# Performance work log

Hardware: AMD Instinct MI355X
Metric: run time of the kernel (lower is better)

## Reference

```python
import jax, jax.numpy as jnp
import numpy as np

OUTPUT_DIM = 64
HIDDEN = 1024
STYLE = 128
SKILL = 128
SEQ_LEN = 256
N_LAYERS = 2
BATCH = 512


def setup_inputs() -> dict:
    key = jax.random.key(0)
    ks = jax.random.split(key, 16)
    s = 0.02
    inp = {
        "z_style": jax.random.normal(ks[0], (BATCH, STYLE), jnp.float32),
        "z_skill": jax.random.normal(ks[1], (BATCH, SKILL), jnp.float32),
        "fc_init_w": jax.random.normal(ks[2], (HIDDEN * N_LAYERS, STYLE + SKILL), jnp.float32) * s,
        "fc_init_b": jnp.zeros((HIDDEN * N_LAYERS,), jnp.float32),
        "W_ih0": jax.random.normal(ks[3], (4 * HIDDEN, OUTPUT_DIM), jnp.float32) * s,
        "W_hh0": jax.random.normal(ks[4], (4 * HIDDEN, HIDDEN), jnp.float32) * s,
        "b_ih0": jnp.zeros((4 * HIDDEN,), jnp.float32),
        "b_hh0": jnp.zeros((4 * HIDDEN,), jnp.float32),
        "W_ih1": jax.random.normal(ks[5], (4 * HIDDEN, HIDDEN), jnp.float32) * s,
        "W_hh1": jax.random.normal(ks[6], (4 * HIDDEN, HIDDEN), jnp.float32) * s,
        "b_ih1": jnp.zeros((4 * HIDDEN,), jnp.float32),
        "b_hh1": jnp.zeros((4 * HIDDEN,), jnp.float32),
        "fc_out_w": jax.random.normal(ks[7], (OUTPUT_DIM, HIDDEN), jnp.float32) * s,
        "fc_out_b": jnp.zeros((OUTPUT_DIM,), jnp.float32),
    }
    return inp


def _lstm_cell(x, h, c, W_ih, W_hh, b_ih, b_hh):
    # PyTorch gate order: i, f, g, o
    gates = x @ W_ih.T + b_ih + h @ W_hh.T + b_hh  # [B, 4H]
    i, f, g, o = jnp.split(gates, 4, axis=-1)
    i = jax.nn.sigmoid(i)
    f = jax.nn.sigmoid(f)
    g = jnp.tanh(g)
    o = jax.nn.sigmoid(o)
    c_new = f * c + i * g
    h_new = o * jnp.tanh(c_new)
    return h_new, c_new


def reference(z_style, z_skill, fc_init_w, fc_init_b, W_ih0, W_hh0, b_ih0, b_hh0,
              W_ih1, W_hh1, b_ih1, b_hh1, fc_out_w, fc_out_b):
    z = jnp.concatenate([z_style, z_skill], axis=1)                # [B, STYLE+SKILL]
    init_flat = z @ fc_init_w.T + fc_init_b                        # [B, n_layers*H]
    # Faithful to torch .view: raw row-major reshape to [n_layers, B, H]
    h0_all = init_flat.reshape(N_LAYERS, -1, HIDDEN)
    c0_all = jnp.zeros_like(h0_all)
    x0 = jnp.zeros((z.shape[0], OUTPUT_DIM), z.dtype)

    def step(carry, _):
        h0, c0, h1, c1, x = carry
        h0, c0 = _lstm_cell(x, h0, c0, W_ih0, W_hh0, b_ih0, b_hh0)
        h1, c1 = _lstm_cell(h0, h1, c1, W_ih1, W_hh1, b_ih1, b_hh1)
        out = h1 @ fc_out_w.T + fc_out_b                           # [B, OUTPUT_DIM]
        return (h0, c0, h1, c1, out), out

    carry0 = (h0_all[0], c0_all[0], h0_all[1], c0_all[1], x0)
    _, outs = jax.lax.scan(step, carry0, None, length=SEQ_LEN)     # [T, B, OUT]
    return jnp.transpose(outs, (1, 0, 2))                          # [B, T, OUT]
```

## Files before the change

### kernel.cpp

```cpp
#include <hip/hip_runtime.h>
#include <hip/hip_bf16.h>
#include <hip/hip_cooperative_groups.h>

#define HID   1024
#define BATCH 512
#define SEQ   256
#define OUTD  64
#define NGATE 4096
#define NBLK  256
#define NTHR  512
#define NPH   512
#define HSZ   (512 * 1024)

typedef __attribute__((ext_vector_type(8))) short bf16x8;
typedef __attribute__((ext_vector_type(4))) float f32x4;
typedef __attribute__((ext_vector_type(16))) float f32x16;
typedef unsigned short u16;
typedef unsigned long long u64;

#define WIN_BYTES 32768
#define LDS_BYTES (2 * WIN_BYTES + 65536)

#define AQ __ATOMIC_RELAXED, __HIP_MEMORY_SCOPE_AGENT

__device__ __forceinline__ u16 f2bf(float v) {
  union { float f; unsigned u; } u; u.f = v;
  unsigned r = u.u + 0x7fffu + ((u.u >> 16) & 1u);
  return (u16)(r >> 16);
}
__device__ __forceinline__ float bf2f(u16 b) {
  union { unsigned u; float f; } u; u.u = ((unsigned)b) << 16;
  return u.f;
}
__device__ __forceinline__ float sigf(float x) { return 1.0f / (1.0f + __expf(-x)); }
__device__ __forceinline__ float tanh_fast(float x) {
  float ax = fabsf(x);
  float e = __expf(-2.0f * ax);
  return copysignf((1.0f - e) / (1.0f + e), x);
}

__device__ __forceinline__ void st_dev32(u16* p, unsigned v) {
  __hip_atomic_store((unsigned*)p, v, AQ);
}
__device__ __forceinline__ u64 ld_dev64(const u16* p) {
  return __hip_atomic_load((const u64*)p, AQ);
}

__device__ __forceinline__ size_t fidx(int np, int k) {
  int s = np >> 5, nl = np & 31;
  int c = k >> 8;
  int kq = (k >> 5) & 7;
  int kfs = (k >> 4) & 1;
  int h = (k >> 3) & 1;
  int e = k & 7;
  int f = c * 2 + kfs;
  return ((size_t)(s * 8 + kq) * 16 + f) * 512 + (h * 32 + nl) * 8 + e;
}


__global__ void k_build_w0f(const float* __restrict__ Whh0, const float* __restrict__ Wih0,
                            const float* __restrict__ fcw, u16* __restrict__ w0f) {
  int np = blockIdx.x;
  int j = np >> 2, gg = np & 3;
  int orig = gg * 1024 + j;
  int tid = threadIdx.x;
  __shared__ float wrow[64];
  if (tid < 64) wrow[tid] = Wih0[orig * 64 + tid];
  __syncthreads();
  for (int k = tid; k < 1024; k += 256) {
    w0f[fidx(np, k)] = f2bf(Whh0[(size_t)orig * 1024 + k]);
    float acc = 0.f;
#pragma unroll
    for (int o = 0; o < 64; ++o) acc += wrow[o] * fcw[o * 1024 + k];
    w0f[fidx(np, 1024 + k)] = f2bf(acc);
  }
}

__global__ void k_build_w1f(const float* __restrict__ Wih1, const float* __restrict__ Whh1,
                            u16* __restrict__ w1f) {
  int np = blockIdx.x;
  int j = np >> 2, gg = np & 3;
  int orig = gg * 1024 + j;
  int tid = threadIdx.x;
  for (int k = tid; k < 1024; k += 256) {
    w1f[fidx(np, k)]        = f2bf(Wih1[(size_t)orig * 1024 + k]);
    w1f[fidx(np, 1024 + k)] = f2bf(Whh1[(size_t)orig * 1024 + k]);
  }
}

__global__ void k_build_bias(const float* bih0, const float* bhh0,
                             const float* bih1, const float* bhh1,
                             const float* Wih0, const float* fcb,
                             float* bias0b, float* bias0x, float* bias1) {
  int np = blockIdx.x * 256 + threadIdx.x;
  if (np >= NGATE) return;
  int j = np >> 2, gg = np & 3;
  int orig = gg * 1024 + j;
  bias0b[np] = bih0[orig] + bhh0[orig];
  bias1[np]  = bih1[orig] + bhh1[orig];
  float acc = 0.f;
#pragma unroll
  for (int o = 0; o < 64; ++o) acc += Wih0[orig * 64 + o] * fcb[o];
  bias0x[np] = acc;
}

__global__ void k_fcwb(const float* __restrict__ fcw, u16* __restrict__ fcwb) {
  int idx = blockIdx.x * 256 + threadIdx.x;
  fcwb[idx] = f2bf(fcw[idx]);
}

__global__ void k_init(const float* __restrict__ zs, const float* __restrict__ zk,
                       const float* __restrict__ fiw, const float* __restrict__ fib,
                       u16* __restrict__ xg0i, u16* __restrict__ xg1i) {
  int r = blockIdx.x;
  int tid = threadIdx.x;
  __shared__ float z[256];
  if (tid < 128) z[tid] = zs[r * 128 + tid];
  else           z[tid] = zk[r * 128 + (tid - 128)];
  __syncthreads();
  for (int c = tid; c < 2048; c += 256) {
    float acc = fib[c];
    const float* w = fiw + (size_t)c * 256;
#pragma unroll 8
    for (int k = 0; k < 256; ++k) acc += z[k] * w[k];
    int l = (r >= 256) ? 1 : 0;
    int b = 2 * (r - l * 256) + (c >> 10);
    int h = c & 1023;
    u16 v = f2bf(acc);
    if (l == 0) xg0i[(size_t)b * 1024 + h] = v;
    else        xg1i[(size_t)b * 1024 + h] = v;
  }
}


struct Params {
  const u16* w0f;
  const u16* w1f;
  const float* bias0b;
  const float* bias0x;
  const float* bias1;
  u16* xg0;
  u16* xg1;
  u16* scr;
  const u16* fcwb;
  const float* fcb;
  float* out;
  unsigned* igctr;
  unsigned* rkg;
  unsigned* gcnt;
  unsigned* sctr;
  unsigned* axg;
  unsigned* rls;
  unsigned* gctr;
};

__global__ __launch_bounds__(NTHR, 2)
void k_lstm(Params p) {
  extern __shared__ char smem[];
  u16* win0 = (u16*)smem;
  u16* win1 = (u16*)(smem + WIN_BYTES);
  float* pld = (float*)(smem + 2 * WIN_BYTES);
  volatile unsigned* bc = (volatile unsigned*)pld;

  const int blk = blockIdx.x, tid = threadIdx.x;
  const int lane = tid & 63, wave = tid >> 6;
  const int x8 = blk & 7;
  const int g = x8 >> 2;
  const int s = (blk >> 3) * 4 + (x8 & 3);
  const int nl = lane & 31, hh = lane >> 5;

  unsigned xcd;
  asm("s_getreg_b32 %0, hwreg(HW_REG_XCC_ID, 0, 32)" : "=s"(xcd));
  xcd &= 7;

  if (tid == 0) {
    unsigned rg = __hip_atomic_fetch_add(&p.rkg[xcd * 2 + g], 1u, AQ);
    __hip_atomic_fetch_add(&p.gcnt[g], 1u, AQ);
    __hip_atomic_fetch_add(p.igctr, 1u, AQ);
    while (__hip_atomic_load(p.igctr, AQ) < (unsigned)NBLK)
      __builtin_amdgcn_s_sleep(2);
    bc[0] = rg;
    bc[1] = __hip_atomic_load(&p.rkg[xcd * 2 + g], AQ);
    bc[2] = __hip_atomic_load(&p.gcnt[g], AQ);
  }
  __syncthreads();
  const unsigned rg_   = bc[0];
  const unsigned ng_   = bc[1];
  const unsigned ngrp_ = bc[2];
  const bool lead = (rg_ == 0);
  __syncthreads();

  bf16x8 w0r[16], w1r[16];
  {
    const u16* W0p = p.w0f + (size_t)(s * 8 + wave) * 8192 + (hh * 32 + nl) * 8;
    const u16* W1p = p.w1f + (size_t)(s * 8 + wave) * 8192 + (hh * 32 + nl) * 8;
#pragma unroll
    for (int f = 0; f < 16; ++f) {
      w0r[f] = *(const bf16x8*)(W0p + f * 512);
      w1r[f] = *(const bf16x8*)(W1p + f * 512);
    }
  }

  const int cr_ = tid >> 3, cj = tid & 7;
  const int npb = s * 32 + 4 * cj;
  const f32x4 b0 = *(const f32x4*)&p.bias0b[npb];
  const f32x4 bx = *(const f32x4*)&p.bias0x[npb];
  const f32x4 b1 = *(const f32x4*)&p.bias1[npb];
  const int jcol = s * 8 + cj;

  float c0s[4] = {0, 0, 0, 0}, c1s[4] = {0, 0, 0, 0};

  u16* scrg = p.scr + (size_t)(xcd * 2 + g) * 256 * 2048;

  auto gbar = [&](int ph) {
    __syncthreads();
    if (tid == 0) {
      unsigned* ax = &p.axg[(xcd * 2 + g) * NPH + ph];
      __hip_atomic_fetch_add(ax, 1u, AQ);
      if (lead) {
        while (__hip_atomic_load(ax, AQ) < ng_) __builtin_amdgcn_s_sleep(1);
        unsigned* gc = &p.gctr[g * NPH + ph];
        __hip_atomic_fetch_add(gc, ng_, AQ);
        while (__hip_atomic_load(gc, AQ) < ngrp_) __builtin_amdgcn_s_sleep(1);
        __hip_atomic_store(&p.rls[(xcd * 2 + g) * NPH + ph], 1u, AQ);
      } else {
        while (!__hip_atomic_load(&p.rls[(xcd * 2 + g) * NPH + ph], AQ))
          __builtin_amdgcn_s_sleep(1);
      }
    }
    __syncthreads();
  };

  auto lbar = [&](int ph) {
    __syncthreads();
    if (tid == 0) {
      unsigned* c = &p.sctr[(xcd * 2 + g) * NPH + ph];
      __hip_atomic_fetch_add(c, 1u, AQ);
      while (__hip_atomic_load(c, AQ) < ng_) __builtin_amdgcn_s_sleep(1);
    }
    __syncthreads();
    asm volatile("buffer_inv sc0\n\ts_waitcnt vmcnt(0)" ::: "memory");
  };

  auto fill = [&](const u16* lo, const u16* hi, bool zhi, bool dohi) {
    const int c = tid;
    for (int r = (int)rg_; r < 256; r += (int)ng_) {
      u16* drow = scrg + (size_t)r * 2048;
      const size_t grow = (size_t)(g * 256 + r) * 1024;
      if (c < 256) {
        *(u64*)(drow + c * 4) = ld_dev64(lo + grow + c * 4);
      } else if (dohi) {
        *(u64*)(drow + 1024 + (c - 256) * 4) =
            zhi ? 0ull : ld_dev64(hi + grow + (c - 256) * 4);
      }
    }
  };

  auto out_proj_s = [&](int tq) {
    const int o = tid >> 3, ks = tid & 7;
#pragma unroll
    for (int rr = 0; rr < 2; ++rr) {
      const int rl = 2 * s + rr;
      const u16* hp = scrg + (size_t)rl * 2048 + 1024 + ks * 128;
      const u16* wp = p.fcwb + (size_t)o * 1024 + ks * 128;
      float a = 0.f;
#pragma unroll
      for (int kk = 0; kk < 128; kk += 8) {
        bf16x8 hv = *(const bf16x8*)(hp + kk);
        bf16x8 wv = *(const bf16x8*)(wp + kk);
#pragma unroll
        for (int jj = 0; jj < 8; ++jj)
          a += bf2f(((u16*)&hv)[jj]) * bf2f(((u16*)&wv)[jj]);
      }
      a += __shfl_xor(a, 1);
      a += __shfl_xor(a, 2);
      a += __shfl_xor(a, 4);
      if (ks == 0)
        p.out[((size_t)(g * 256 + rl) * SEQ + tq) * OUTD + o] = a + p.fcb[o];
    }
  };

  auto phase = [&](bf16x8 (&wr)[16], u16* dst,
                   const f32x4& bb, const f32x4& bxx, bool ubx, float (&cs)[4]) {
#pragma unroll
    for (int pass = 0; pass < 4; ++pass) {
      const u16* Xb = scrg + (size_t)(pass * 64) * 2048;
      f32x16 acc0, acc1;
#pragma unroll
      for (int z = 0; z < 16; ++z) { acc0[z] = 0.f; acc1[z] = 0.f; }

      {
        const int row = tid >> 3, seg = tid & 7, sw = (row & 7) << 4;
        const u16* src = Xb + (size_t)row * 2048 + seg * 8;
#pragma unroll
        for (int i = 0; i < 4; ++i)
          *(bf16x8*)(win0 + row * 256 + (((seg * 16 + i * 128) ^ sw) >> 1)) =
              *(const bf16x8*)(src + i * 64);
      }
      __syncthreads();
#pragma unroll
      for (int c = 0; c < 8; ++c) {
        u16* cur = (c & 1) ? win1 : win0;
        u16* nxt = (c & 1) ? win0 : win1;
        if (c < 7) {
          const int row = tid >> 3, seg = tid & 7, sw = (row & 7) << 4;
          const u16* src = Xb + (size_t)row * 2048 + (c + 1) * 256 + seg * 8;
#pragma unroll
          for (int i = 0; i < 4; ++i)
            *(bf16x8*)(nxt + row * 256 + (((seg * 16 + i * 128) ^ sw) >> 1)) =
                *(const bf16x8*)(src + i * 64);
        }
#pragma unroll
        for (int kfs = 0; kfs < 2; ++kfs) {
          const bf16x8 wf = wr[c * 2 + kfs];
          const int bo = wave * 64 + kfs * 32 + hh * 16;
          {
            const int row = nl;
            const bf16x8 a =
                *(const bf16x8*)(cur + row * 256 + ((bo ^ ((row & 7) << 4)) >> 1));
            acc0 = __builtin_amdgcn_mfma_f32_32x32x16_bf16(a, wf, acc0, 0, 0, 0);
          }
          {
            const int row = 32 + nl;
            const bf16x8 a =
                *(const bf16x8*)(cur + row * 256 + ((bo ^ ((row & 7) << 4)) >> 1));
            acc1 = __builtin_amdgcn_mfma_f32_32x32x16_bf16(a, wf, acc1, 0, 0, 0);
          }
        }
        __syncthreads();
      }
#pragma unroll
      for (int r16 = 0; r16 < 16; ++r16) {
        const int row0 = (r16 & 3) + 8 * (r16 >> 2) + 4 * hh;
        pld[(wave * 64 + row0) * 32 + nl] = acc0[r16];
        pld[(wave * 64 + 32 + row0) * 32 + nl] = acc1[r16];
      }
      __syncthreads();
      f32x4 gs = {0.f, 0.f, 0.f, 0.f};
#pragma unroll
      for (int q = 0; q < 8; ++q) {
        const f32x4 v = *(const f32x4*)&pld[(q * 64 + cr_) * 32 + 4 * cj];
        gs[0] += v[0]; gs[1] += v[1]; gs[2] += v[2]; gs[3] += v[3];
      }
      const float gi = gs[0] + bb[0] + (ubx ? bxx[0] : 0.f);
      const float gf = gs[1] + bb[1] + (ubx ? bxx[1] : 0.f);
      const float gg = gs[2] + bb[2] + (ubx ? bxx[2] : 0.f);
      const float go = gs[3] + bb[3] + (ubx ? bxx[3] : 0.f);
      const float iv = sigf(gi), fv = sigf(gf), gv = tanh_fast(gg), ov = sigf(go);
      const float cnew = fv * cs[pass] + iv * gv;
      cs[pass] = cnew;
      const float hnew = ov * tanh_fast(cnew);
      const u16 hv = f2bf(hnew);
      const unsigned other = __shfl_xor((unsigned)hv, 1);
      if (!(tid & 1)) {
        const unsigned pairv = (unsigned)hv | (other << 16);
        st_dev32(dst + (size_t)(g * 256 + pass * 64 + cr_) * 1024 + jcol, pairv);
      }
      __syncthreads();
    }
  };

  for (int t = 0; t < SEQ; ++t) {
    const int pp = t & 1, pq = pp ^ 1;
    const int ph = 2 * t;
    fill(p.xg0 + (size_t)pq * HSZ, p.xg1 + (size_t)pq * HSZ, t == 0, true);
    lbar(ph);
    if (t > 0) out_proj_s(t - 1);
    phase(w0r, p.xg0 + (size_t)pp * HSZ, b0, bx, t > 0, c0s);
    gbar(ph);
    fill(p.xg0 + (size_t)pp * HSZ, p.xg1 + (size_t)pq * HSZ, false, t == 0);
    lbar(ph + 1);
    phase(w1r, p.xg1 + (size_t)pp * HSZ, b1, b1, false, c1s);
    gbar(ph + 1);
  }
  {
    const u16* h1b = p.xg1 + (size_t)((SEQ - 1) & 1) * HSZ;
    const int o = tid >> 3, ks = tid & 7;
#pragma unroll
    for (int rr = 0; rr < 2; ++rr) {
      const int r = g * 256 + 2 * s + rr;
      const u16* hp = h1b + (size_t)r * 1024 + ks * 128;
      const u16* wp = p.fcwb + (size_t)o * 1024 + ks * 128;
      float a = 0.f;
      for (int kk = 0; kk < 128; kk += 4) {
        u64 hv = ld_dev64(hp + kk);
        a += bf2f((u16)hv)         * bf2f(wp[kk]);
        a += bf2f((u16)(hv >> 16)) * bf2f(wp[kk + 1]);
        a += bf2f((u16)(hv >> 32)) * bf2f(wp[kk + 2]);
        a += bf2f((u16)(hv >> 48)) * bf2f(wp[kk + 3]);
      }
      a += __shfl_xor(a, 1);
      a += __shfl_xor(a, 2);
      a += __shfl_xor(a, 4);
      if (ks == 0)
        p.out[((size_t)r * SEQ + (SEQ - 1)) * OUTD + o] = a + p.fcb[o];
    }
  }
}


extern "C" void kernel_launch(void* const* d_in, const int* in_sizes, int n_in,
                              void* d_out, int out_size, void* d_ws, size_t ws_size,
                              hipStream_t stream) {
  const float* zs   = (const float*)d_in[0];
  const float* zk   = (const float*)d_in[1];
  const float* fiw  = (const float*)d_in[2];
  const float* fib  = (const float*)d_in[3];
  const float* Wih0 = (const float*)d_in[4];
  const float* Whh0 = (const float*)d_in[5];
  const float* bih0 = (const float*)d_in[6];
  const float* bhh0 = (const float*)d_in[7];
  const float* Wih1 = (const float*)d_in[8];
  const float* Whh1 = (const float*)d_in[9];
  const float* bih1 = (const float*)d_in[10];
  const float* bhh1 = (const float*)d_in[11];
  const float* fcw  = (const float*)d_in[12];
  const float* fcb  = (const float*)d_in[13];
  float* out = (float*)d_out;

  char* ws = (char*)d_ws;
  size_t off = 0;
  auto alloc = [&](size_t bytes) -> char* {
    char* pp = ws + off;
    off += (bytes + 255) & ~(size_t)255;
    return pp;
  };
  u16* w0f  = (u16*)alloc((size_t)NGATE * 2048 * 2);
  u16* w1f  = (u16*)alloc((size_t)NGATE * 2048 * 2);
  u16* xg0  = (u16*)alloc((size_t)2 * HSZ * 2);
  u16* xg1  = (u16*)alloc((size_t)2 * HSZ * 2);
  u16* scr  = (u16*)alloc((size_t)8 * 2 * 256 * 2048 * 2);
  u16* fcwb = (u16*)alloc((size_t)OUTD * HID * 2);
  float* bias0b = (float*)alloc(NGATE * 4);
  float* bias0x = (float*)alloc(NGATE * 4);
  float* bias1  = (float*)alloc(NGATE * 4);
  unsigned* igctr = (unsigned*)alloc(256);
  unsigned* rkg   = (unsigned*)alloc(16 * 4);
  unsigned* gcnt  = (unsigned*)alloc(2 * 4);
  unsigned* sctr  = (unsigned*)alloc((size_t)16 * NPH * 4);
  unsigned* axg   = (unsigned*)alloc((size_t)16 * NPH * 4);
  unsigned* rls   = (unsigned*)alloc((size_t)16 * NPH * 4);
  unsigned* gctr  = (unsigned*)alloc((size_t)2 * NPH * 4);

  hipMemsetAsync(igctr, 0, 256, stream);
  hipMemsetAsync(rkg, 0, 16 * 4, stream);
  hipMemsetAsync(gcnt, 0, 2 * 4, stream);
  hipMemsetAsync(sctr, 0, (size_t)16 * NPH * 4, stream);
  hipMemsetAsync(axg, 0, (size_t)16 * NPH * 4, stream);
  hipMemsetAsync(rls, 0, (size_t)16 * NPH * 4, stream);
  hipMemsetAsync(gctr, 0, (size_t)2 * NPH * 4, stream);

  hipLaunchKernelGGL(k_build_w0f, dim3(NGATE), dim3(256), 0, stream, Whh0, Wih0, fcw, w0f);
  hipLaunchKernelGGL(k_build_w1f, dim3(NGATE), dim3(256), 0, stream, Wih1, Whh1, w1f);
  hipLaunchKernelGGL(k_build_bias, dim3(16), dim3(256), 0, stream,
                     bih0, bhh0, bih1, bhh1, Wih0, fcb, bias0b, bias0x, bias1);
  hipLaunchKernelGGL(k_fcwb, dim3(256), dim3(256), 0, stream, fcw, fcwb);
  hipLaunchKernelGGL(k_init, dim3(BATCH), dim3(256), 0, stream, zs, zk, fiw, fib,
                     xg0 + (size_t)1 * HSZ, xg1 + (size_t)1 * HSZ);

  Params prm;
  prm.w0f = w0f; prm.w1f = w1f;
  prm.bias0b = bias0b; prm.bias0x = bias0x; prm.bias1 = bias1;
  prm.xg0 = xg0; prm.xg1 = xg1; prm.scr = scr;
  prm.fcwb = fcwb; prm.fcb = fcb; prm.out = out;
  prm.igctr = igctr; prm.rkg = rkg; prm.gcnt = gcnt;
  prm.sctr = sctr; prm.axg = axg; prm.rls = rls; prm.gctr = gctr;

  hipFuncSetAttribute((const void*)k_lstm, hipFuncAttributeMaxDynamicSharedMemorySize, LDS_BYTES);
  void* args[] = { &prm };
  hipLaunchCooperativeKernel((void*)k_lstm, dim3(NBLK), dim3(NTHR), args, LDS_BYTES, stream);
}
```

Measured before the change: 22.23 ms.

## Drop LDS staging windows, read MFMA operands from scratch directly, single-buffer hidden state

Removes the double-buffered LDS window staging in the gate GEMM, so MFMA A-operands are loaded straight from the per-XCD scratch buffer and the per-chunk __syncthreads go away. The hidden-state buffers become single instead of ping-pong, and the fill step is split into per-layer halves using 16-byte loads marked sc0 sc1 with batched waits. The barrier schedule is reordered so each layer refreshes only the half it needs. The risks are higher global/L2 latency on MFMA operand fetches and write-after-read hazards on the now single-buffered state.

```diff
diff --git a/kernel.cpp b/kernel.cpp
--- a/kernel.cpp
+++ b/kernel.cpp
@@ -10,16 +10,17 @@
 #define NBLK  256
 #define NTHR  512
 #define NPH   512
+#define NLB   520
 #define HSZ   (512 * 1024)
 
 typedef __attribute__((ext_vector_type(8))) short bf16x8;
 typedef __attribute__((ext_vector_type(4))) float f32x4;
 typedef __attribute__((ext_vector_type(16))) float f32x16;
+typedef __attribute__((ext_vector_type(4))) unsigned u32x4;
 typedef unsigned short u16;
 typedef unsigned long long u64;
 
-#define WIN_BYTES 32768
-#define LDS_BYTES (2 * WIN_BYTES + 65536)
+#define LDS_BYTES (65536 + 256)
 
 #define AQ __ATOMIC_RELAXED, __HIP_MEMORY_SCOPE_AGENT
 
@@ -45,6 +46,10 @@
 __device__ __forceinline__ u64 ld_dev64(const u16* p) {
   return __hip_atomic_load((const u64*)p, AQ);
 }
+
+#define LD_BYP16(dst, addr) \
+  asm volatile("global_load_dwordx4 %0, %1, off sc0 sc1" \
+               : "=v"(dst) : "v"(addr) : "memory")
 
 __device__ __forceinline__ size_t fidx(int np, int k) {
   int s = np >> 5, nl = np & 31;
@@ -111,7 +116,7 @@
 
 __global__ void k_init(const float* __restrict__ zs, const float* __restrict__ zk,
                        const float* __restrict__ fiw, const float* __restrict__ fib,
-                       u16* __restrict__ xg0i, u16* __restrict__ xg1i) {
+                       u16* __restrict__ xg0, u16* __restrict__ xg1) {
   int r = blockIdx.x;
   int tid = threadIdx.x;
   __shared__ float z[256];
@@ -127,8 +132,8 @@
     int b = 2 * (r - l * 256) + (c >> 10);
     int h = c & 1023;
     u16 v = f2bf(acc);
-    if (l == 0) xg0i[(size_t)b * 1024 + h] = v;
-    else        xg1i[(size_t)b * 1024 + h] = v;
+    if (l == 0) xg0[(size_t)b * 1024 + h] = v;
+    else        xg1[(size_t)b * 1024 + h] = v;
   }
 }
 
@@ -157,10 +162,8 @@
 __global__ __launch_bounds__(NTHR, 2)
 void k_lstm(Params p) {
   extern __shared__ char smem[];
-  u16* win0 = (u16*)smem;
-  u16* win1 = (u16*)(smem + WIN_BYTES);
-  float* pld = (float*)(smem + 2 * WIN_BYTES);
-  volatile unsigned* bc = (volatile unsigned*)pld;
+  float* pld = (float*)smem;
+  volatile unsigned* bc = (volatile unsigned*)(smem + 65536);
 
   const int blk = blockIdx.x, tid = threadIdx.x;
   const int lane = tid & 63, wave = tid >> 6;
@@ -231,10 +234,10 @@
     __syncthreads();
   };
 
-  auto lbar = [&](int ph) {
+  auto lbar = [&](int slot) {
     __syncthreads();
     if (tid == 0) {
-      unsigned* c = &p.sctr[(xcd * 2 + g) * NPH + ph];
+      unsigned* c = &p.sctr[(xcd * 2 + g) * NLB + slot];
       __hip_atomic_fetch_add(c, 1u, AQ);
       while (__hip_atomic_load(c, AQ) < ng_) __builtin_amdgcn_s_sleep(1);
     }
@@ -242,17 +245,25 @@
     asm volatile("buffer_inv sc0\n\ts_waitcnt vmcnt(0)" ::: "memory");
   };
 
-  auto fill = [&](const u16* lo, const u16* hi, bool zhi, bool dohi) {
-    const int c = tid;
-    for (int r = (int)rg_; r < 256; r += (int)ng_) {
-      u16* drow = scrg + (size_t)r * 2048;
-      const size_t grow = (size_t)(g * 256 + r) * 1024;
-      if (c < 256) {
-        *(u64*)(drow + c * 4) = ld_dev64(lo + grow + c * 4);
-      } else if (dohi) {
-        *(u64*)(drow + 1024 + (c - 256) * 4) =
-            zhi ? 0ull : ld_dev64(hi + grow + (c - 256) * 4);
-      }
+  auto fill_half = [&](const u16* src, int off, bool zero) {
+    const int rsub = tid >> 7;
+    const int csub = (tid & 127) * 8;
+    for (int c0 = (int)rg_; c0 < 64; c0 += 4 * (int)ng_) {
+      const int c1 = c0 + (int)ng_, c2 = c0 + 2 * (int)ng_, c3 = c0 + 3 * (int)ng_;
+      u32x4 v0 = {0,0,0,0}, v1 = {0,0,0,0}, v2 = {0,0,0,0}, v3 = {0,0,0,0};
+      if (!zero) {
+        LD_BYP16(v0, src + (size_t)(g * 256 + c0 * 4 + rsub) * 1024 + csub);
+        if (c1 < 64) LD_BYP16(v1, src + (size_t)(g * 256 + c1 * 4 + rsub) * 1024 + csub);
+        if (c2 < 64) LD_BYP16(v2, src + (size_t)(g * 256 + c2 * 4 + rsub) * 1024 + csub);
+        if (c3 < 64) LD_BYP16(v3, src + (size_t)(g * 256 + c3 * 4 + rsub) * 1024 + csub);
+        asm volatile("s_waitcnt vmcnt(0)"
+                     : "+v"(v0), "+v"(v1), "+v"(v2), "+v"(v3) :: "memory");
+        __builtin_amdgcn_sched_barrier(0);
+      }
+      *(u32x4*)(scrg + (size_t)(c0 * 4 + rsub) * 2048 + off + csub) = v0;
+      if (c1 < 64) *(u32x4*)(scrg + (size_t)(c1 * 4 + rsub) * 2048 + off + csub) = v1;
+      if (c2 < 64) *(u32x4*)(scrg + (size_t)(c2 * 4 + rsub) * 2048 + off + csub) = v2;
+      if (c3 < 64) *(u32x4*)(scrg + (size_t)(c3 * 4 + rsub) * 2048 + off + csub) = v3;
     }
   };
 
@@ -284,50 +295,21 @@
                    const f32x4& bb, const f32x4& bxx, bool ubx, float (&cs)[4]) {
 #pragma unroll
     for (int pass = 0; pass < 4; ++pass) {
-      const u16* Xb = scrg + (size_t)(pass * 64) * 2048;
+      const u16* b0p = scrg + (size_t)(pass * 64 + nl) * 2048 + wave * 32 + hh * 8;
+      const u16* b1p = b0p + (size_t)32 * 2048;
       f32x16 acc0, acc1;
 #pragma unroll
       for (int z = 0; z < 16; ++z) { acc0[z] = 0.f; acc1[z] = 0.f; }
-
-      {
-        const int row = tid >> 3, seg = tid & 7, sw = (row & 7) << 4;
-        const u16* src = Xb + (size_t)row * 2048 + seg * 8;
-#pragma unroll
-        for (int i = 0; i < 4; ++i)
-          *(bf16x8*)(win0 + row * 256 + (((seg * 16 + i * 128) ^ sw) >> 1)) =
-              *(const bf16x8*)(src + i * 64);
-      }
-      __syncthreads();
 #pragma unroll
       for (int c = 0; c < 8; ++c) {
-        u16* cur = (c & 1) ? win1 : win0;
-        u16* nxt = (c & 1) ? win0 : win1;
-        if (c < 7) {
-          const int row = tid >> 3, seg = tid & 7, sw = (row & 7) << 4;
-          const u16* src = Xb + (size_t)row * 2048 + (c + 1) * 256 + seg * 8;
-#pragma unroll
-          for (int i = 0; i < 4; ++i)
-            *(bf16x8*)(nxt + row * 256 + (((seg * 16 + i * 128) ^ sw) >> 1)) =
-                *(const bf16x8*)(src + i * 64);
-        }
-#pragma unroll
-        for (int kfs = 0; kfs < 2; ++kfs) {
-          const bf16x8 wf = wr[c * 2 + kfs];
-          const int bo = wave * 64 + kfs * 32 + hh * 16;
-          {
-            const int row = nl;
-            const bf16x8 a =
-                *(const bf16x8*)(cur + row * 256 + ((bo ^ ((row & 7) << 4)) >> 1));
-            acc0 = __builtin_amdgcn_mfma_f32_32x32x16_bf16(a, wf, acc0, 0, 0, 0);
-          }
-          {
-            const int row = 32 + nl;
-            const bf16x8 a =
-                *(const bf16x8*)(cur + row * 256 + ((bo ^ ((row & 7) << 4)) >> 1));
-            acc1 = __builtin_amdgcn_mfma_f32_32x32x16_bf16(a, wf, acc1, 0, 0, 0);
-          }
-        }
-        __syncthreads();
+        const bf16x8 f0 = *(const bf16x8*)(b0p + c * 256);
+        const bf16x8 f1 = *(const bf16x8*)(b0p + c * 256 + 16);
+        const bf16x8 f2 = *(const bf16x8*)(b1p + c * 256);
+        const bf16x8 f3 = *(const bf16x8*)(b1p + c * 256 + 16);
+        acc0 = __builtin_amdgcn_mfma_f32_32x32x16_bf16(f0, wr[2 * c],     acc0, 0, 0, 0);
+        acc0 = __builtin_amdgcn_mfma_f32_32x32x16_bf16(f1, wr[2 * c + 1], acc0, 0, 0, 0);
+        acc1 = __builtin_amdgcn_mfma_f32_32x32x16_bf16(f2, wr[2 * c],     acc1, 0, 0, 0);
+        acc1 = __builtin_amdgcn_mfma_f32_32x32x16_bf16(f3, wr[2 * c + 1], acc1, 0, 0, 0);
       }
 #pragma unroll
       for (int r16 = 0; r16 < 16; ++r16) {
@@ -360,26 +342,30 @@
     }
   };
 
+  fill_half(p.xg0, 0, false);
+  fill_half(nullptr, 1024, true);
+  lbar(0);
+
   for (int t = 0; t < SEQ; ++t) {
-    const int pp = t & 1, pq = pp ^ 1;
-    const int ph = 2 * t;
-    fill(p.xg0 + (size_t)pq * HSZ, p.xg1 + (size_t)pq * HSZ, t == 0, true);
-    lbar(ph);
     if (t > 0) out_proj_s(t - 1);
-    phase(w0r, p.xg0 + (size_t)pp * HSZ, b0, bx, t > 0, c0s);
-    gbar(ph);
-    fill(p.xg0 + (size_t)pp * HSZ, p.xg1 + (size_t)pq * HSZ, false, t == 0);
-    lbar(ph + 1);
-    phase(w1r, p.xg1 + (size_t)pp * HSZ, b1, b1, false, c1s);
-    gbar(ph + 1);
+    phase(w0r, p.xg0, b0, bx, t > 0, c0s);
+    gbar(2 * t);
+    fill_half(p.xg0, 0, false);
+    if (t == 0) fill_half(p.xg1, 1024, false);
+    lbar(2 * t + 1);
+    phase(w1r, p.xg1, b1, b1, false, c1s);
+    gbar(2 * t + 1);
+    if (t + 1 < SEQ) {
+      fill_half(p.xg1, 1024, false);
+      lbar(2 * t + 2);
+    }
   }
   {
-    const u16* h1b = p.xg1 + (size_t)((SEQ - 1) & 1) * HSZ;
     const int o = tid >> 3, ks = tid & 7;
 #pragma unroll
     for (int rr = 0; rr < 2; ++rr) {
       const int r = g * 256 + 2 * s + rr;
-      const u16* hp = h1b + (size_t)r * 1024 + ks * 128;
+      const u16* hp = p.xg1 + (size_t)r * 1024 + ks * 128;
       const u16* wp = p.fcwb + (size_t)o * 1024 + ks * 128;
       float a = 0.f;
       for (int kk = 0; kk < 128; kk += 4) {
@@ -427,8 +413,8 @@
   };
   u16* w0f  = (u16*)alloc((size_t)NGATE * 2048 * 2);
   u16* w1f  = (u16*)alloc((size_t)NGATE * 2048 * 2);
-  u16* xg0  = (u16*)alloc((size_t)2 * HSZ * 2);
-  u16* xg1  = (u16*)alloc((size_t)2 * HSZ * 2);
+  u16* xg0  = (u16*)alloc((size_t)HSZ * 2);
+  u16* xg1  = (u16*)alloc((size_t)HSZ * 2);
   u16* scr  = (u16*)alloc((size_t)8 * 2 * 256 * 2048 * 2);
   u16* fcwb = (u16*)alloc((size_t)OUTD * HID * 2);
   float* bias0b = (float*)alloc(NGATE * 4);
@@ -437,7 +423,7 @@
   unsigned* igctr = (unsigned*)alloc(256);
   unsigned* rkg   = (unsigned*)alloc(16 * 4);
   unsigned* gcnt  = (unsigned*)alloc(2 * 4);
-  unsigned* sctr  = (unsigned*)alloc((size_t)16 * NPH * 4);
+  unsigned* sctr  = (unsigned*)alloc((size_t)16 * NLB * 4);
   unsigned* axg   = (unsigned*)alloc((size_t)16 * NPH * 4);
   unsigned* rls   = (unsigned*)alloc((size_t)16 * NPH * 4);
   unsigned* gctr  = (unsigned*)alloc((size_t)2 * NPH * 4);
@@ -445,7 +431,7 @@
   hipMemsetAsync(igctr, 0, 256, stream);
   hipMemsetAsync(rkg, 0, 16 * 4, stream);
   hipMemsetAsync(gcnt, 0, 2 * 4, stream);
-  hipMemsetAsync(sctr, 0, (size_t)16 * NPH * 4, stream);
+  hipMemsetAsync(sctr, 0, (size_t)16 * NLB * 4, stream);
   hipMemsetAsync(axg, 0, (size_t)16 * NPH * 4, stream);
   hipMemsetAsync(rls, 0, (size_t)16 * NPH * 4, stream);
   hipMemsetAsync(gctr, 0, (size_t)2 * NPH * 4, stream);
@@ -455,8 +441,7 @@
   hipLaunchKernelGGL(k_build_bias, dim3(16), dim3(256), 0, stream,
                      bih0, bhh0, bih1, bhh1, Wih0, fcb, bias0b, bias0x, bias1);
   hipLaunchKernelGGL(k_fcwb, dim3(256), dim3(256), 0, stream, fcw, fcwb);
-  hipLaunchKernelGGL(k_init, dim3(BATCH), dim3(256), 0, stream, zs, zk, fiw, fib,
-                     xg0 + (size_t)1 * HSZ, xg1 + (size_t)1 * HSZ);
+  hipLaunchKernelGGL(k_init, dim3(BATCH), dim3(256), 0, stream, zs, zk, fiw, fib, xg0, xg1);
 
   Params prm;
   prm.w0f = w0f; prm.w1f = w1f;
```

After: 35.65 ms. 1.6x slower.

## Single-buffer hidden states and move layer-1 fill after phase barrier

Applied to the files above, without the earlier changes.

Drops the double-buffered xg0/xg1 hidden-state arrays in favour of single buffers. The per-block scratch fill is restructured so each half is copied right after the phase that produced it, and the fill loop is batched with eight independent loads in flight per thread. This reorders the per-step schedule, so the first fill and local barrier move out of the loop. It also resizes the local-barrier counter array and moves the broadcast LDS slot so it no longer aliases pld. The aim is fewer redundant copies and more memory-level parallelism in the fill, at the risk of read-after-write hazards on the now-shared single buffers.

```diff
diff --git a/kernel.cpp b/kernel.cpp
--- a/kernel.cpp
+++ b/kernel.cpp
@@ -10,6 +10,7 @@
 #define NBLK  256
 #define NTHR  512
 #define NPH   512
+#define NLB   520
 #define HSZ   (512 * 1024)
 
 typedef __attribute__((ext_vector_type(8))) short bf16x8;
@@ -19,7 +20,7 @@
 typedef unsigned long long u64;
 
 #define WIN_BYTES 32768
-#define LDS_BYTES (2 * WIN_BYTES + 65536)
+#define LDS_BYTES (2 * WIN_BYTES + 65536 + 256)
 
 #define AQ __ATOMIC_RELAXED, __HIP_MEMORY_SCOPE_AGENT
 
@@ -111,7 +112,7 @@
 
 __global__ void k_init(const float* __restrict__ zs, const float* __restrict__ zk,
                        const float* __restrict__ fiw, const float* __restrict__ fib,
-                       u16* __restrict__ xg0i, u16* __restrict__ xg1i) {
+                       u16* __restrict__ xg0, u16* __restrict__ xg1) {
   int r = blockIdx.x;
   int tid = threadIdx.x;
   __shared__ float z[256];
@@ -127,8 +128,8 @@
     int b = 2 * (r - l * 256) + (c >> 10);
     int h = c & 1023;
     u16 v = f2bf(acc);
-    if (l == 0) xg0i[(size_t)b * 1024 + h] = v;
-    else        xg1i[(size_t)b * 1024 + h] = v;
+    if (l == 0) xg0[(size_t)b * 1024 + h] = v;
+    else        xg1[(size_t)b * 1024 + h] = v;
   }
 }
 
@@ -160,7 +161,7 @@
   u16* win0 = (u16*)smem;
   u16* win1 = (u16*)(smem + WIN_BYTES);
   float* pld = (float*)(smem + 2 * WIN_BYTES);
-  volatile unsigned* bc = (volatile unsigned*)pld;
+  volatile unsigned* bc = (volatile unsigned*)(smem + 2 * WIN_BYTES + 65536);
 
   const int blk = blockIdx.x, tid = threadIdx.x;
   const int lane = tid & 63, wave = tid >> 6;
@@ -231,10 +232,10 @@
     __syncthreads();
   };
 
-  auto lbar = [&](int ph) {
+  auto lbar = [&](int slot) {
     __syncthreads();
     if (tid == 0) {
-      unsigned* c = &p.sctr[(xcd * 2 + g) * NPH + ph];
+      unsigned* c = &p.sctr[(xcd * 2 + g) * NLB + slot];
       __hip_atomic_fetch_add(c, 1u, AQ);
       while (__hip_atomic_load(c, AQ) < ng_) __builtin_amdgcn_s_sleep(1);
     }
@@ -242,17 +243,24 @@
     asm volatile("buffer_inv sc0\n\ts_waitcnt vmcnt(0)" ::: "memory");
   };
 
-  auto fill = [&](const u16* lo, const u16* hi, bool zhi, bool dohi) {
-    const int c = tid;
-    for (int r = (int)rg_; r < 256; r += (int)ng_) {
-      u16* drow = scrg + (size_t)r * 2048;
-      const size_t grow = (size_t)(g * 256 + r) * 1024;
-      if (c < 256) {
-        *(u64*)(drow + c * 4) = ld_dev64(lo + grow + c * 4);
-      } else if (dohi) {
-        *(u64*)(drow + 1024 + (c - 256) * 4) =
-            zhi ? 0ull : ld_dev64(hi + grow + (c - 256) * 4);
-      }
+  auto fill_half = [&](const u16* src, int off, bool zero) {
+    const int half = tid >> 8;
+    const int c8 = (tid & 255) * 4;
+    for (int kb = 0; (int)rg_ + kb * (int)ng_ < 256; kb += 16) {
+      u64 v[8];
+      int rr[8];
+#pragma unroll
+      for (int it = 0; it < 8; ++it) {
+        const int k = kb + it * 2 + half;
+        rr[it] = (int)rg_ + k * (int)ng_;
+        v[it] = 0;
+        if (!zero && rr[it] < 256)
+          v[it] = ld_dev64(src + (size_t)(g * 256 + rr[it]) * 1024 + c8);
+      }
+#pragma unroll
+      for (int it = 0; it < 8; ++it)
+        if (rr[it] < 256)
+          *(u64*)(scrg + (size_t)rr[it] * 2048 + off + c8) = v[it];
     }
   };
 
@@ -360,26 +368,30 @@
     }
   };
 
+  fill_half(p.xg0, 0, false);
+  fill_half(nullptr, 1024, true);
+  lbar(0);
+
   for (int t = 0; t < SEQ; ++t) {
-    const int pp = t & 1, pq = pp ^ 1;
-    const int ph = 2 * t;
-    fill(p.xg0 + (size_t)pq * HSZ, p.xg1 + (size_t)pq * HSZ, t == 0, true);
-    lbar(ph);
     if (t > 0) out_proj_s(t - 1);
-    phase(w0r, p.xg0 + (size_t)pp * HSZ, b0, bx, t > 0, c0s);
-    gbar(ph);
-    fill(p.xg0 + (size_t)pp * HSZ, p.xg1 + (size_t)pq * HSZ, false, t == 0);
-    lbar(ph + 1);
-    phase(w1r, p.xg1 + (size_t)pp * HSZ, b1, b1, false, c1s);
-    gbar(ph + 1);
+    phase(w0r, p.xg0, b0, bx, t > 0, c0s);
+    gbar(2 * t);
+    fill_half(p.xg0, 0, false);
+    if (t == 0) fill_half(p.xg1, 1024, false);
+    lbar(2 * t + 1);
+    phase(w1r, p.xg1, b1, b1, false, c1s);
+    gbar(2 * t + 1);
+    if (t + 1 < SEQ) {
+      fill_half(p.xg1, 1024, false);
+      lbar(2 * t + 2);
+    }
   }
   {
-    const u16* h1b = p.xg1 + (size_t)((SEQ - 1) & 1) * HSZ;
     const int o = tid >> 3, ks = tid & 7;
 #pragma unroll
     for (int rr = 0; rr < 2; ++rr) {
       const int r = g * 256 + 2 * s + rr;
-      const u16* hp = h1b + (size_t)r * 1024 + ks * 128;
+      const u16* hp = p.xg1 + (size_t)r * 1024 + ks * 128;
       const u16* wp = p.fcwb + (size_t)o * 1024 + ks * 128;
       float a = 0.f;
       for (int kk = 0; kk < 128; kk += 4) {
@@ -427,8 +439,8 @@
   };
   u16* w0f  = (u16*)alloc((size_t)NGATE * 2048 * 2);
   u16* w1f  = (u16*)alloc((size_t)NGATE * 2048 * 2);
-  u16* xg0  = (u16*)alloc((size_t)2 * HSZ * 2);
-  u16* xg1  = (u16*)alloc((size_t)2 * HSZ * 2);
+  u16* xg0  = (u16*)alloc((size_t)HSZ * 2);
+  u16* xg1  = (u16*)alloc((size_t)HSZ * 2);
   u16* scr  = (u16*)alloc((size_t)8 * 2 * 256 * 2048 * 2);
   u16* fcwb = (u16*)alloc((size_t)OUTD * HID * 2);
   float* bias0b = (float*)alloc(NGATE * 4);
@@ -437,7 +449,7 @@
   unsigned* igctr = (unsigned*)alloc(256);
   unsigned* rkg   = (unsigned*)alloc(16 * 4);
   unsigned* gcnt  = (unsigned*)alloc(2 * 4);
-  unsigned* sctr  = (unsigned*)alloc((size_t)16 * NPH * 4);
+  unsigned* sctr  = (unsigned*)alloc((size_t)16 * NLB * 4);
   unsigned* axg   = (unsigned*)alloc((size_t)16 * NPH * 4);
   unsigned* rls   = (unsigned*)alloc((size_t)16 * NPH * 4);
   unsigned* gctr  = (unsigned*)alloc((size_t)2 * NPH * 4);
@@ -445,7 +457,7 @@
   hipMemsetAsync(igctr, 0, 256, stream);
   hipMemsetAsync(rkg, 0, 16 * 4, stream);
   hipMemsetAsync(gcnt, 0, 2 * 4, stream);
-  hipMemsetAsync(sctr, 0, (size_t)16 * NPH * 4, stream);
+  hipMemsetAsync(sctr, 0, (size_t)16 * NLB * 4, stream);
   hipMemsetAsync(axg, 0, (size_t)16 * NPH * 4, stream);
   hipMemsetAsync(rls, 0, (size_t)16 * NPH * 4, stream);
   hipMemsetAsync(gctr, 0, (size_t)2 * NPH * 4, stream);
@@ -455,8 +467,7 @@
   hipLaunchKernelGGL(k_build_bias, dim3(16), dim3(256), 0, stream,
                      bih0, bhh0, bih1, bhh1, Wih0, fcb, bias0b, bias0x, bias1);
   hipLaunchKernelGGL(k_fcwb, dim3(256), dim3(256), 0, stream, fcw, fcwb);
-  hipLaunchKernelGGL(k_init, dim3(BATCH), dim3(256), 0, stream, zs, zk, fiw, fib,
-                     xg0 + (size_t)1 * HSZ, xg1 + (size_t)1 * HSZ);
+  hipLaunchKernelGGL(k_init, dim3(BATCH), dim3(256), 0, stream, zs, zk, fiw, fib, xg0, xg1);
 
   Params prm;
   prm.w0f = w0f; prm.w1f = w1f;
```

After: 25.55 ms. 15.0% more time.
